# Kernel tuning notes

Hardware: AMD Instinct MI355X
Metric: run time of the kernel (lower is better)

Reference implementation:

```python
import jax, jax.numpy as jnp
import numpy as np

B, T, H, L = 512, 128, 768, 12
START, STOP = 9, 10
NEG = -10000.0


def setup_inputs() -> dict:
    key = jax.random.key(0)
    k1, k2, k3, k4 = jax.random.split(key, 4)
    bert_seq_out = jax.random.normal(k1, (B, T, H), dtype=jnp.float32)
    label_ids = jax.random.randint(k2, (B, T), 0, L, dtype=jnp.int64)
    # hidden2label: xavier_uniform weight, zero bias
    limit = float(np.sqrt(6.0 / (H + L)))
    W = jax.random.uniform(k3, (L, H), minval=-limit, maxval=limit, dtype=jnp.float32)
    b = jnp.zeros((L,), dtype=jnp.float32)
    # transitions ~ randn, with start row / stop column masked to -10000
    transitions = jax.random.normal(k4, (L, L), dtype=jnp.float32)
    transitions = transitions.at[START, :].set(NEG)
    transitions = transitions.at[:, STOP].set(NEG)
    return {"bert_seq_out": bert_seq_out, "W": W, "b": b,
            "transitions": transitions, "label_ids": label_ids}


def _crf_nll(bert_seq_out, W, b, transitions, label_ids):
    # hidden2label projection (dropout omitted: eval-mode identity)
    feats = jnp.einsum('bth,lh->btl', bert_seq_out, W) + b  # [B,T,L]
    Bx = feats.shape[0]

    # ---- forward (alpha) recursion in log domain ----
    log_alpha0 = jnp.full((Bx, L), NEG, dtype=feats.dtype).at[:, START].set(0.0)
    feats_t = jnp.transpose(feats, (1, 0, 2))  # [T,B,L]

    def step(log_alpha, feat_t):
        # logsumexp over previous label: transitions[next, prev] + alpha[prev]
        scores = transitions[None, :, :] + log_alpha[:, None, :]  # [B,L(next),L(prev)]
        new = jax.scipy.special.logsumexp(scores, axis=-1) + feat_t
        return new, None

    log_alpha, _ = jax.lax.scan(step, log_alpha0, feats_t[1:])
    forward_score = jax.scipy.special.logsumexp(log_alpha, axis=-1)  # [B]

    # ---- gold path score ----
    prev, nxt = label_ids[:, :-1], label_ids[:, 1:]  # [B,T-1]
    trans_score = transitions[nxt, prev].sum(axis=-1)  # [B]
    emit_score = jnp.take_along_axis(feats[:, 1:], nxt[..., None], axis=-1)[..., 0].sum(axis=-1)
    gold_score = trans_score + emit_score  # [B]

    return jnp.mean(forward_score - gold_score)


def reference(bert_seq_out, W, b, transitions, label_ids):
    return _crf_nll(bert_seq_out, W, b, transitions, label_ids)
```

## Files before the change

kernel.cpp:

```cpp
#include <hip/hip_runtime.h>


#define Bsz 512
#define Tt  128
#define Hh  768
#define Ll  12
#define START_TAG 9
#define NEGV -10000.0f

__global__ __launch_bounds__(256) void feats_kernel(
    const float* __restrict__ X, const float* __restrict__ W,
    const float* __restrict__ bias, float* __restrict__ feats)
{
  __shared__ float sW[Ll * Hh];
  __shared__ float sB[Ll];
  const int tid = threadIdx.x;

  for (int i = tid; i < Ll * Hh / 4; i += 256)
    reinterpret_cast<float4*>(sW)[i] = reinterpret_cast<const float4*>(W)[i];
  if (tid < Ll) sB[tid] = bias[tid];
  __syncthreads();

  float sbr[Ll];
#pragma unroll
  for (int l = 0; l < Ll; ++l) sbr[l] = sB[l];

  const int gidx = tid >> 4;
  const int j    = tid & 15;
  const int row0 = blockIdx.x * 32 + gidx * 2;
  const int row1 = row0 + 1;

  const float* x0 = X + (size_t)row0 * Hh;
  const float* x1 = X + (size_t)row1 * Hh;

  float acc0[Ll], acc1[Ll];
#pragma unroll
  for (int l = 0; l < Ll; ++l) { acc0[l] = 0.f; acc1[l] = 0.f; }

#pragma unroll
  for (int it = 0; it < Hh / 64; ++it) {
    const int h = 4 * j + 64 * it;
    const float4 xa = *reinterpret_cast<const float4*>(x0 + h);
    const float4 xb = *reinterpret_cast<const float4*>(x1 + h);
#pragma unroll
    for (int l = 0; l < Ll; ++l) {
      const float4 wv = *reinterpret_cast<const float4*>(sW + l * Hh + h);
      acc0[l] += xa.x * wv.x + xa.y * wv.y + xa.z * wv.z + xa.w * wv.w;
      acc1[l] += xb.x * wv.x + xb.y * wv.y + xb.z * wv.z + xb.w * wv.w;
    }
  }

#pragma unroll
  for (int l = 0; l < Ll; ++l) {
#pragma unroll
    for (int d = 1; d < 16; d <<= 1) {
      acc0[l] += __shfl_xor(acc0[l], d, 16);
      acc1[l] += __shfl_xor(acc1[l], d, 16);
    }
  }

  if (j == 0) {
    float* o0 = feats + (size_t)row0 * Ll;
    float* o1 = feats + (size_t)row1 * Ll;
    *reinterpret_cast<float4*>(o0 + 0) = make_float4(acc0[0]+sbr[0], acc0[1]+sbr[1], acc0[2]+sbr[2],  acc0[3]+sbr[3]);
    *reinterpret_cast<float4*>(o0 + 4) = make_float4(acc0[4]+sbr[4], acc0[5]+sbr[5], acc0[6]+sbr[6],  acc0[7]+sbr[7]);
    *reinterpret_cast<float4*>(o0 + 8) = make_float4(acc0[8]+sbr[8], acc0[9]+sbr[9], acc0[10]+sbr[10],acc0[11]+sbr[11]);
    *reinterpret_cast<float4*>(o1 + 0) = make_float4(acc1[0]+sbr[0], acc1[1]+sbr[1], acc1[2]+sbr[2],  acc1[3]+sbr[3]);
    *reinterpret_cast<float4*>(o1 + 4) = make_float4(acc1[4]+sbr[4], acc1[5]+sbr[5], acc1[6]+sbr[6],  acc1[7]+sbr[7]);
    *reinterpret_cast<float4*>(o1 + 8) = make_float4(acc1[8]+sbr[8], acc1[9]+sbr[9], acc1[10]+sbr[10],acc1[11]+sbr[11]);
  }
}

#define FSTRIDE 1544
__global__ __launch_bounds__(64) void crf_kernel(
    const float* __restrict__ feats, const float* __restrict__ trans,
    const int* __restrict__ labels, float* __restrict__ bscores)
{
  __shared__ float sf[4 * FSTRIDE];
  __shared__ float st[Ll * Ll];
  const int tid = threadIdx.x;
  const int g   = tid >> 4;
  const int j   = tid & 15;
  const int batch0 = blockIdx.x * 4;

  for (int i = tid; i < Ll * Ll; i += 64) st[i] = trans[i];
  for (int g2 = 0; g2 < 4; ++g2) {
    const float4* src = reinterpret_cast<const float4*>(
        feats + (size_t)(batch0 + g2) * (Tt * Ll));
    float4* dst = reinterpret_cast<float4*>(sf + g2 * FSTRIDE);
    for (int i = tid; i < Tt * Ll / 4; i += 64) dst[i] = src[i];
  }
  __syncthreads();

  float E[Ll];
#pragma unroll
  for (int k = 0; k < Ll; ++k) E[k] = 0.f;
  if (j < Ll) {
#pragma unroll
    for (int k = 0; k < Ll; ++k) E[k] = __expf(st[j * Ll + k]);
  }

  const float* fme = sf + g * FSTRIDE;
  float alpha = (j == START_TAG) ? 0.0f : NEGV;

  for (int t = 1; t < Tt; ++t) {
    float m = alpha;
#pragma unroll
    for (int d = 8; d >= 1; d >>= 1) m = fmaxf(m, __shfl_xor(m, d, 16));
    const float p = __expf(alpha - m);
    float s = 0.f;
#pragma unroll
    for (int k = 0; k < Ll; ++k) s = fmaf(E[k], __shfl(p, k, 16), s);
    const float anew = m + __logf(s) + fme[t * Ll + j];
    alpha = (j < Ll) ? anew : NEGV;
  }

  float m = alpha;
#pragma unroll
  for (int d = 8; d >= 1; d >>= 1) m = fmaxf(m, __shfl_xor(m, d, 16));
  float p = __expf(alpha - m);
#pragma unroll
  for (int d = 8; d >= 1; d >>= 1) p += __shfl_xor(p, d, 16);
  const float fwd = m + __logf(p);

  const int* lab = labels + (size_t)(batch0 + g) * Tt;
  float gs = 0.f;
  for (int t = j; t < Tt - 1; t += 16) {
    const int pv = lab[t], nx = lab[t + 1];
    gs += st[nx * Ll + pv] + fme[(t + 1) * Ll + nx];
  }
#pragma unroll
  for (int d = 8; d >= 1; d >>= 1) gs += __shfl_xor(gs, d, 16);

  if (j == 0) bscores[batch0 + g] = fwd - gs;
}

__global__ __launch_bounds__(64) void reduce_kernel(
    const float* __restrict__ bs, float* __restrict__ out)
{
  const int tid = threadIdx.x;
  float s = 0.f;
  for (int i = tid; i < Bsz; i += 64) s += bs[i];
#pragma unroll
  for (int d = 32; d >= 1; d >>= 1) s += __shfl_xor(s, d, 64);
  if (tid == 0) out[0] = s * (1.0f / Bsz);
}

extern "C" void kernel_launch(void* const* d_in, const int* in_sizes, int n_in,
                              void* d_out, int out_size, void* d_ws, size_t ws_size,
                              hipStream_t stream) {
  const float* X     = (const float*)d_in[0];
  const float* W     = (const float*)d_in[1];
  const float* b     = (const float*)d_in[2];
  const float* trans = (const float*)d_in[3];
  const int*   lab   = (const int*)d_in[4];
  float* out = (float*)d_out;

  float* feats   = (float*)d_ws;
  float* bscores = feats + (size_t)Bsz * Tt * Ll;

  feats_kernel<<<(Bsz * Tt) / 32, 256, 0, stream>>>(X, W, b, feats);
  crf_kernel<<<Bsz / 4, 64, 0, stream>>>(feats, trans, lab, bscores);
  reduce_kernel<<<1, 64, 0, stream>>>(bscores, out);
}
```

Baseline: 361.7 us.

## Normalize CRF alpha by label-0 score and process four rows per group in projection

The projection kernel now has each 16-lane group compute four rows instead of two, so each shared-memory weight load is reused across more rows and the grid is halved. The CRF recursion drops the per-step max shuffle reduction. Instead it renormalizes alpha relative to the label-0 score, computed redundantly in every lane, and accumulates that offset in a scalar. This shortens the serial dependency chain per time step. In exchange it costs more registers in both kernels, and without a true max there is some risk of exp overflow or underflow if the label-0 score drifts far from the others.

```diff
diff --git a/kernel.cpp b/kernel.cpp
--- a/kernel.cpp
+++ b/kernel.cpp
@@ -21,32 +21,33 @@
   if (tid < Ll) sB[tid] = bias[tid];
   __syncthreads();
 
-  float sbr[Ll];
-#pragma unroll
-  for (int l = 0; l < Ll; ++l) sbr[l] = sB[l];
-
   const int gidx = tid >> 4;
   const int j    = tid & 15;
-  const int row0 = blockIdx.x * 32 + gidx * 2;
-  const int row1 = row0 + 1;
+  const int row0 = blockIdx.x * 64 + gidx * 4;
 
   const float* x0 = X + (size_t)row0 * Hh;
-  const float* x1 = X + (size_t)row1 * Hh;
+  const float* x1 = x0 + Hh;
+  const float* x2 = x1 + Hh;
+  const float* x3 = x2 + Hh;
 
-  float acc0[Ll], acc1[Ll];
+  float acc0[Ll], acc1[Ll], acc2[Ll], acc3[Ll];
 #pragma unroll
-  for (int l = 0; l < Ll; ++l) { acc0[l] = 0.f; acc1[l] = 0.f; }
+  for (int l = 0; l < Ll; ++l) { acc0[l]=0.f; acc1[l]=0.f; acc2[l]=0.f; acc3[l]=0.f; }
 
 #pragma unroll
   for (int it = 0; it < Hh / 64; ++it) {
     const int h = 4 * j + 64 * it;
     const float4 xa = *reinterpret_cast<const float4*>(x0 + h);
     const float4 xb = *reinterpret_cast<const float4*>(x1 + h);
+    const float4 xc = *reinterpret_cast<const float4*>(x2 + h);
+    const float4 xd = *reinterpret_cast<const float4*>(x3 + h);
 #pragma unroll
     for (int l = 0; l < Ll; ++l) {
       const float4 wv = *reinterpret_cast<const float4*>(sW + l * Hh + h);
-      acc0[l] += xa.x * wv.x + xa.y * wv.y + xa.z * wv.z + xa.w * wv.w;
-      acc1[l] += xb.x * wv.x + xb.y * wv.y + xb.z * wv.z + xb.w * wv.w;
+      acc0[l] += xa.x*wv.x + xa.y*wv.y + xa.z*wv.z + xa.w*wv.w;
+      acc1[l] += xb.x*wv.x + xb.y*wv.y + xb.z*wv.z + xb.w*wv.w;
+      acc2[l] += xc.x*wv.x + xc.y*wv.y + xc.z*wv.z + xc.w*wv.w;
+      acc3[l] += xd.x*wv.x + xd.y*wv.y + xd.z*wv.z + xd.w*wv.w;
     }
   }
 
@@ -56,18 +57,28 @@
     for (int d = 1; d < 16; d <<= 1) {
       acc0[l] += __shfl_xor(acc0[l], d, 16);
       acc1[l] += __shfl_xor(acc1[l], d, 16);
+      acc2[l] += __shfl_xor(acc2[l], d, 16);
+      acc3[l] += __shfl_xor(acc3[l], d, 16);
     }
   }
 
   if (j == 0) {
-    float* o0 = feats + (size_t)row0 * Ll;
-    float* o1 = feats + (size_t)row1 * Ll;
-    *reinterpret_cast<float4*>(o0 + 0) = make_float4(acc0[0]+sbr[0], acc0[1]+sbr[1], acc0[2]+sbr[2],  acc0[3]+sbr[3]);
-    *reinterpret_cast<float4*>(o0 + 4) = make_float4(acc0[4]+sbr[4], acc0[5]+sbr[5], acc0[6]+sbr[6],  acc0[7]+sbr[7]);
-    *reinterpret_cast<float4*>(o0 + 8) = make_float4(acc0[8]+sbr[8], acc0[9]+sbr[9], acc0[10]+sbr[10],acc0[11]+sbr[11]);
-    *reinterpret_cast<float4*>(o1 + 0) = make_float4(acc1[0]+sbr[0], acc1[1]+sbr[1], acc1[2]+sbr[2],  acc1[3]+sbr[3]);
-    *reinterpret_cast<float4*>(o1 + 4) = make_float4(acc1[4]+sbr[4], acc1[5]+sbr[5], acc1[6]+sbr[6],  acc1[7]+sbr[7]);
-    *reinterpret_cast<float4*>(o1 + 8) = make_float4(acc1[8]+sbr[8], acc1[9]+sbr[9], acc1[10]+sbr[10],acc1[11]+sbr[11]);
+    float* o = feats + (size_t)row0 * Ll;
+    *reinterpret_cast<float4*>(o + 0) = make_float4(acc0[0]+sB[0], acc0[1]+sB[1], acc0[2]+sB[2],  acc0[3]+sB[3]);
+    *reinterpret_cast<float4*>(o + 4) = make_float4(acc0[4]+sB[4], acc0[5]+sB[5], acc0[6]+sB[6],  acc0[7]+sB[7]);
+    *reinterpret_cast<float4*>(o + 8) = make_float4(acc0[8]+sB[8], acc0[9]+sB[9], acc0[10]+sB[10],acc0[11]+sB[11]);
+    o += Ll;
+    *reinterpret_cast<float4*>(o + 0) = make_float4(acc1[0]+sB[0], acc1[1]+sB[1], acc1[2]+sB[2],  acc1[3]+sB[3]);
+    *reinterpret_cast<float4*>(o + 4) = make_float4(acc1[4]+sB[4], acc1[5]+sB[5], acc1[6]+sB[6],  acc1[7]+sB[7]);
+    *reinterpret_cast<float4*>(o + 8) = make_float4(acc1[8]+sB[8], acc1[9]+sB[9], acc1[10]+sB[10],acc1[11]+sB[11]);
+    o += Ll;
+    *reinterpret_cast<float4*>(o + 0) = make_float4(acc2[0]+sB[0], acc2[1]+sB[1], acc2[2]+sB[2],  acc2[3]+sB[3]);
+    *reinterpret_cast<float4*>(o + 4) = make_float4(acc2[4]+sB[4], acc2[5]+sB[5], acc2[6]+sB[6],  acc2[7]+sB[7]);
+    *reinterpret_cast<float4*>(o + 8) = make_float4(acc2[8]+sB[8], acc2[9]+sB[9], acc2[10]+sB[10],acc2[11]+sB[11]);
+    o += Ll;
+    *reinterpret_cast<float4*>(o + 0) = make_float4(acc3[0]+sB[0], acc3[1]+sB[1], acc3[2]+sB[2],  acc3[3]+sB[3]);
+    *reinterpret_cast<float4*>(o + 4) = make_float4(acc3[4]+sB[4], acc3[5]+sB[5], acc3[6]+sB[6],  acc3[7]+sB[7]);
+    *reinterpret_cast<float4*>(o + 8) = make_float4(acc3[8]+sB[8], acc3[9]+sB[9], acc3[10]+sB[10],acc3[11]+sB[11]);
   }
 }
 
@@ -81,6 +92,7 @@
   const int tid = threadIdx.x;
   const int g   = tid >> 4;
   const int j   = tid & 15;
+  const int jj  = (j < Ll) ? j : (Ll - 1);
   const int batch0 = blockIdx.x * 4;
 
   for (int i = tid; i < Ll * Ll; i += 64) st[i] = trans[i];
@@ -92,36 +104,46 @@
   }
   __syncthreads();
 
-  float E[Ll];
+  float E[Ll], E0[Ll];
 #pragma unroll
-  for (int k = 0; k < Ll; ++k) E[k] = 0.f;
-  if (j < Ll) {
-#pragma unroll
-    for (int k = 0; k < Ll; ++k) E[k] = __expf(st[j * Ll + k]);
+  for (int k = 0; k < Ll; ++k) {
+    E[k]  = __expf(st[jj * Ll + k]);
+    E0[k] = __expf(st[k]);
   }
 
   const float* fme = sf + g * FSTRIDE;
-  float alpha = (j == START_TAG) ? 0.0f : NEGV;
+  float beta = (j == START_TAG) ? 0.0f : NEGV;
+  float c = 0.0f;
 
   for (int t = 1; t < Tt; ++t) {
-    float m = alpha;
+    const float p = __expf(beta);
+    float ph[Ll];
 #pragma unroll
-    for (int d = 8; d >= 1; d >>= 1) m = fmaxf(m, __shfl_xor(m, d, 16));
-    const float p = __expf(alpha - m);
-    float s = 0.f;
+    for (int k = 0; k < Ll; ++k) ph[k] = __shfl(p, k, 16);
+    float sa = 0.f, sb = 0.f, sc = 0.f, za = 0.f, zb = 0.f, zc = 0.f;
 #pragma unroll
-    for (int k = 0; k < Ll; ++k) s = fmaf(E[k], __shfl(p, k, 16), s);
-    const float anew = m + __logf(s) + fme[t * Ll + j];
-    alpha = (j < Ll) ? anew : NEGV;
+    for (int k = 0; k < Ll; k += 3) {
+      sa = fmaf(E[k],    ph[k],   sa);  za = fmaf(E0[k],    ph[k],   za);
+      sb = fmaf(E[k+1],  ph[k+1], sb);  zb = fmaf(E0[k+1],  ph[k+1], zb);
+      sc = fmaf(E[k+2],  ph[k+2], sc);  zc = fmaf(E0[k+2],  ph[k+2], zc);
+    }
+    const float s  = (sa + sb) + sc;
+    const float s0 = (za + zb) + zc;
+    const float fj = fme[t * Ll + jj];
+    const float f0 = fme[t * Ll];
+    const float a0 = __logf(s0) + f0;
+    beta = (__logf(s) + fj) - a0;
+    c += a0;
   }
 
-  float m = alpha;
+  float bv = (j < Ll) ? beta : NEGV;
+  float m = bv;
 #pragma unroll
   for (int d = 8; d >= 1; d >>= 1) m = fmaxf(m, __shfl_xor(m, d, 16));
-  float p = __expf(alpha - m);
+  float p = __expf(bv - m);
 #pragma unroll
   for (int d = 8; d >= 1; d >>= 1) p += __shfl_xor(p, d, 16);
-  const float fwd = m + __logf(p);
+  const float fwd = c + m + __logf(p);
 
   const int* lab = labels + (size_t)(batch0 + g) * Tt;
   float gs = 0.f;
@@ -159,7 +181,7 @@
   float* feats   = (float*)d_ws;
   float* bscores = feats + (size_t)Bsz * Tt * Ll;
 
-  feats_kernel<<<(Bsz * Tt) / 32, 256, 0, stream>>>(X, W, b, feats);
+  feats_kernel<<<(Bsz * Tt) / 64, 256, 0, stream>>>(X, W, b, feats);
   crf_kernel<<<Bsz / 4, 64, 0, stream>>>(feats, trans, lab, bscores);
   reduce_kernel<<<1, 64, 0, stream>>>(bscores, out);
 }
```

Measured after the change: 337.3 us. -6.7%, faster.

## Fuse projection and CRF into per-batch kernel with cheaper normalized recursion

Applied to the files above, without the earlier changes.

Merges the emission projection and CRF forward/gold-score kernels into one kernel with one block per sequence, keeping emissions in shared memory instead of a global round trip. Each thread group now computes eight rows to reuse weight loads from shared memory. The forward recursion replaces the per-step max reduction with normalization by the label-0 score, shortening the serial dependency chain. This trades occupancy and register pressure, and has only 16 active threads during the recursion, for fewer launches and less traffic.

```diff
diff --git a/kernel.cpp b/kernel.cpp
--- a/kernel.cpp
+++ b/kernel.cpp
@@ -8,131 +8,123 @@
 #define START_TAG 9
 #define NEGV -10000.0f
 
-__global__ __launch_bounds__(256) void feats_kernel(
+__global__ __launch_bounds__(256) void fused_kernel(
     const float* __restrict__ X, const float* __restrict__ W,
-    const float* __restrict__ bias, float* __restrict__ feats)
+    const float* __restrict__ bias, const float* __restrict__ trans,
+    const int* __restrict__ labels, float* __restrict__ bscores)
 {
   __shared__ float sW[Ll * Hh];
+  __shared__ float sT[Ll * Ll];
   __shared__ float sB[Ll];
+  __shared__ float sF[Tt * Ll];
+  __shared__ float sFwd, sGold;
+
   const int tid = threadIdx.x;
+  const int b   = blockIdx.x;
 
   for (int i = tid; i < Ll * Hh / 4; i += 256)
     reinterpret_cast<float4*>(sW)[i] = reinterpret_cast<const float4*>(W)[i];
-  if (tid < Ll) sB[tid] = bias[tid];
+  if (tid < Ll * Ll) sT[tid] = trans[tid];
+  if (tid < Ll)      sB[tid] = bias[tid];
   __syncthreads();
 
-  float sbr[Ll];
+  const int g = tid >> 4;
+  const int j = tid & 15;
+  const int row0 = g * 8;
+  const float* xb = X + ((size_t)b * Tt + row0) * Hh;
+
+  float acc[8][Ll];
 #pragma unroll
-  for (int l = 0; l < Ll; ++l) sbr[l] = sB[l];
+  for (int r = 0; r < 8; ++r)
+#pragma unroll
+    for (int l = 0; l < Ll; ++l) acc[r][l] = 0.f;
 
-  const int gidx = tid >> 4;
-  const int j    = tid & 15;
-  const int row0 = blockIdx.x * 32 + gidx * 2;
-  const int row1 = row0 + 1;
-
-  const float* x0 = X + (size_t)row0 * Hh;
-  const float* x1 = X + (size_t)row1 * Hh;
-
-  float acc0[Ll], acc1[Ll];
-#pragma unroll
-  for (int l = 0; l < Ll; ++l) { acc0[l] = 0.f; acc1[l] = 0.f; }
-
-#pragma unroll
+#pragma unroll 2
   for (int it = 0; it < Hh / 64; ++it) {
     const int h = 4 * j + 64 * it;
-    const float4 xa = *reinterpret_cast<const float4*>(x0 + h);
-    const float4 xb = *reinterpret_cast<const float4*>(x1 + h);
+    float4 xv[8];
+#pragma unroll
+    for (int r = 0; r < 8; ++r)
+      xv[r] = *reinterpret_cast<const float4*>(xb + r * Hh + h);
 #pragma unroll
     for (int l = 0; l < Ll; ++l) {
       const float4 wv = *reinterpret_cast<const float4*>(sW + l * Hh + h);
-      acc0[l] += xa.x * wv.x + xa.y * wv.y + xa.z * wv.z + xa.w * wv.w;
-      acc1[l] += xb.x * wv.x + xb.y * wv.y + xb.z * wv.z + xb.w * wv.w;
+#pragma unroll
+      for (int r = 0; r < 8; ++r)
+        acc[r][l] += xv[r].x*wv.x + xv[r].y*wv.y + xv[r].z*wv.z + xv[r].w*wv.w;
     }
   }
 
 #pragma unroll
-  for (int l = 0; l < Ll; ++l) {
+  for (int r = 0; r < 8; ++r)
 #pragma unroll
-    for (int d = 1; d < 16; d <<= 1) {
-      acc0[l] += __shfl_xor(acc0[l], d, 16);
-      acc1[l] += __shfl_xor(acc1[l], d, 16);
-    }
-  }
+    for (int l = 0; l < Ll; ++l)
+#pragma unroll
+      for (int d = 1; d < 16; d <<= 1)
+        acc[r][l] += __shfl_xor(acc[r][l], d, 16);
 
   if (j == 0) {
-    float* o0 = feats + (size_t)row0 * Ll;
-    float* o1 = feats + (size_t)row1 * Ll;
-    *reinterpret_cast<float4*>(o0 + 0) = make_float4(acc0[0]+sbr[0], acc0[1]+sbr[1], acc0[2]+sbr[2],  acc0[3]+sbr[3]);
-    *reinterpret_cast<float4*>(o0 + 4) = make_float4(acc0[4]+sbr[4], acc0[5]+sbr[5], acc0[6]+sbr[6],  acc0[7]+sbr[7]);
-    *reinterpret_cast<float4*>(o0 + 8) = make_float4(acc0[8]+sbr[8], acc0[9]+sbr[9], acc0[10]+sbr[10],acc0[11]+sbr[11]);
-    *reinterpret_cast<float4*>(o1 + 0) = make_float4(acc1[0]+sbr[0], acc1[1]+sbr[1], acc1[2]+sbr[2],  acc1[3]+sbr[3]);
-    *reinterpret_cast<float4*>(o1 + 4) = make_float4(acc1[4]+sbr[4], acc1[5]+sbr[5], acc1[6]+sbr[6],  acc1[7]+sbr[7]);
-    *reinterpret_cast<float4*>(o1 + 8) = make_float4(acc1[8]+sbr[8], acc1[9]+sbr[9], acc1[10]+sbr[10],acc1[11]+sbr[11]);
-  }
-}
-
-#define FSTRIDE 1544
-__global__ __launch_bounds__(64) void crf_kernel(
-    const float* __restrict__ feats, const float* __restrict__ trans,
-    const int* __restrict__ labels, float* __restrict__ bscores)
-{
-  __shared__ float sf[4 * FSTRIDE];
-  __shared__ float st[Ll * Ll];
-  const int tid = threadIdx.x;
-  const int g   = tid >> 4;
-  const int j   = tid & 15;
-  const int batch0 = blockIdx.x * 4;
-
-  for (int i = tid; i < Ll * Ll; i += 64) st[i] = trans[i];
-  for (int g2 = 0; g2 < 4; ++g2) {
-    const float4* src = reinterpret_cast<const float4*>(
-        feats + (size_t)(batch0 + g2) * (Tt * Ll));
-    float4* dst = reinterpret_cast<float4*>(sf + g2 * FSTRIDE);
-    for (int i = tid; i < Tt * Ll / 4; i += 64) dst[i] = src[i];
+#pragma unroll
+    for (int r = 0; r < 8; ++r) {
+      float* o = sF + (row0 + r) * Ll;
+      *reinterpret_cast<float4*>(o + 0) = make_float4(acc[r][0]+sB[0], acc[r][1]+sB[1], acc[r][2]+sB[2],  acc[r][3]+sB[3]);
+      *reinterpret_cast<float4*>(o + 4) = make_float4(acc[r][4]+sB[4], acc[r][5]+sB[5], acc[r][6]+sB[6],  acc[r][7]+sB[7]);
+      *reinterpret_cast<float4*>(o + 8) = make_float4(acc[r][8]+sB[8], acc[r][9]+sB[9], acc[r][10]+sB[10],acc[r][11]+sB[11]);
+    }
   }
   __syncthreads();
 
-  float E[Ll];
+  if (tid < 16) {
+    const int jj = (tid < Ll) ? tid : (Ll - 1);
+    float E[Ll], E0[Ll];
 #pragma unroll
-  for (int k = 0; k < Ll; ++k) E[k] = 0.f;
-  if (j < Ll) {
+    for (int k = 0; k < Ll; ++k) {
+      E[k]  = __expf(sT[jj * Ll + k]);
+      E0[k] = __expf(sT[k]);
+    }
+    float beta = (tid == START_TAG) ? 0.0f : NEGV;
+    float c = 0.0f;
+    for (int t = 1; t < Tt; ++t) {
+      const float p = __expf(beta);
+      float ph[Ll];
 #pragma unroll
-    for (int k = 0; k < Ll; ++k) E[k] = __expf(st[j * Ll + k]);
-  }
-
-  const float* fme = sf + g * FSTRIDE;
-  float alpha = (j == START_TAG) ? 0.0f : NEGV;
-
-  for (int t = 1; t < Tt; ++t) {
-    float m = alpha;
+      for (int k = 0; k < Ll; ++k) ph[k] = __shfl(p, k, 16);
+      float sa = 0.f, sb = 0.f, sc = 0.f, za = 0.f, zb = 0.f, zc = 0.f;
+#pragma unroll
+      for (int k = 0; k < Ll; k += 3) {
+        sa = fmaf(E[k],   ph[k],   sa);  za = fmaf(E0[k],   ph[k],   za);
+        sb = fmaf(E[k+1], ph[k+1], sb);  zb = fmaf(E0[k+1], ph[k+1], zb);
+        sc = fmaf(E[k+2], ph[k+2], sc);  zc = fmaf(E0[k+2], ph[k+2], zc);
+      }
+      const float s  = (sa + sb) + sc;
+      const float s0 = (za + zb) + zc;
+      const float a0 = __logf(s0) + sF[t * Ll];
+      beta = (__logf(s) + sF[t * Ll + jj]) - a0;
+      c += a0;
+    }
+    float bv = (tid < Ll) ? beta : NEGV;
+    float m = bv;
 #pragma unroll
     for (int d = 8; d >= 1; d >>= 1) m = fmaxf(m, __shfl_xor(m, d, 16));
-    const float p = __expf(alpha - m);
-    float s = 0.f;
+    float p = __expf(bv - m);
 #pragma unroll
-    for (int k = 0; k < Ll; ++k) s = fmaf(E[k], __shfl(p, k, 16), s);
-    const float anew = m + __logf(s) + fme[t * Ll + j];
-    alpha = (j < Ll) ? anew : NEGV;
+    for (int d = 8; d >= 1; d >>= 1) p += __shfl_xor(p, d, 16);
+    if (tid == 0) sFwd = c + m + __logf(p);
+  } else if (tid >= 64 && tid < 128) {
+    const int lane = tid - 64;
+    const int* lab = labels + (size_t)b * Tt;
+    float gs = 0.f;
+    for (int t = lane; t < Tt - 1; t += 64) {
+      const int pv = lab[t], nx = lab[t + 1];
+      gs += sT[nx * Ll + pv] + sF[(t + 1) * Ll + nx];
+    }
+#pragma unroll
+    for (int d = 32; d >= 1; d >>= 1) gs += __shfl_xor(gs, d, 64);
+    if (lane == 0) sGold = gs;
   }
+  __syncthreads();
 
-  float m = alpha;
-#pragma unroll
-  for (int d = 8; d >= 1; d >>= 1) m = fmaxf(m, __shfl_xor(m, d, 16));
-  float p = __expf(alpha - m);
-#pragma unroll
-  for (int d = 8; d >= 1; d >>= 1) p += __shfl_xor(p, d, 16);
-  const float fwd = m + __logf(p);
-
-  const int* lab = labels + (size_t)(batch0 + g) * Tt;
-  float gs = 0.f;
-  for (int t = j; t < Tt - 1; t += 16) {
-    const int pv = lab[t], nx = lab[t + 1];
-    gs += st[nx * Ll + pv] + fme[(t + 1) * Ll + nx];
-  }
-#pragma unroll
-  for (int d = 8; d >= 1; d >>= 1) gs += __shfl_xor(gs, d, 16);
-
-  if (j == 0) bscores[batch0 + g] = fwd - gs;
+  if (tid == 0) bscores[b] = sFwd - sGold;
 }
 
 __global__ __launch_bounds__(64) void reduce_kernel(
@@ -156,10 +148,8 @@
   const int*   lab   = (const int*)d_in[4];
   float* out = (float*)d_out;
 
-  float* feats   = (float*)d_ws;
-  float* bscores = feats + (size_t)Bsz * Tt * Ll;
+  float* bscores = (float*)d_ws;
 
-  feats_kernel<<<(Bsz * Tt) / 32, 256, 0, stream>>>(X, W, b, feats);
-  crf_kernel<<<Bsz / 4, 64, 0, stream>>>(feats, trans, lab, bscores);
+  fused_kernel<<<Bsz, 256, 0, stream>>>(X, W, b, trans, lab, bscores);
   reduce_kernel<<<1, 64, 0, stream>>>(bscores, out);
 }
```

Result: faster. 334.2 us (-7.6%).
